# Optimization experiments

Measured on AMD Instinct MI355X. Metric: run time of the kernel, lower is better.

## Reference

```python
import jax, jax.numpy as jnp
import numpy as np

K = 24  # number of clusters (all ids in [0,K) assumed present per image)
DELTA_VAR = 1.0
DELTA_DIST = 2.0
VAR_W = 1.0
DIST_W = 1.0
REG_W = 1.0


def setup_inputs() -> dict:
    key = jax.random.key(0)
    k1, k2 = jax.random.split(key)
    data = jax.random.normal(k1, (4, 16, 512, 1024), dtype=jnp.float32)
    labels = jax.random.randint(k2, (4, 512, 1024), 0, K, dtype=jnp.int32)
    return {"data": data, "labels": labels}


def reference(data, labels):
    B, D, H, Wd = data.shape
    N = H * Wd
    # [B, N, D] points, [B*N] global segment ids (batch-offset cluster ids)
    X = jnp.transpose(data.reshape(B, D, N), (0, 2, 1)).reshape(B * N, D)
    seg = (labels.reshape(B, N) + jnp.arange(B, dtype=labels.dtype)[:, None] * K).reshape(-1)

    # per-cluster sums and counts -> centers  [B*K, D]
    sums = jax.ops.segment_sum(X, seg, num_segments=B * K)
    counts = jax.ops.segment_sum(jnp.ones((B * N,), X.dtype), seg, num_segments=B * K)
    centers_flat = sums / counts[:, None]
    centers = centers_flat.reshape(B, K, D)
    counts_bk = counts.reshape(B, K)

    # variance term: per-point hinged distance to own cluster center
    c_per_point = centers_flat[seg]                      # [B*N, D]
    pt_dist = jnp.linalg.norm(X - c_per_point, axis=1)   # [B*N]
    hv = jnp.maximum(pt_dist - DELTA_VAR, 0.0) ** 2
    var_per_cluster = jax.ops.segment_sum(hv, seg, num_segments=B * K).reshape(B, K) / counts_bk
    var_sum = var_per_cluster.sum()

    # distance term: pairwise center distances (diagonal kept, as in original,
    # contributing a constant delta_dist**2 per cluster)
    diff = centers[:, :, None, :] - centers[:, None, :, :]     # [B, K, K, D]
    sq = jnp.sum(diff * diff, axis=-1)                         # [B, K, K]
    eye = jnp.eye(K, dtype=bool)[None]
    cdist = jnp.where(eye, 0.0, jnp.sqrt(jnp.where(eye, 1.0, sq)))
    hd = jnp.maximum(DELTA_DIST - cdist, 0.0) ** 2
    dist_sum = hd.sum() / (2.0 * K * (K - 1))

    # regularization: mean center norm per image, summed over batch
    reg_sum = jnp.linalg.norm(centers, axis=2).mean(axis=1).sum()

    loss = (VAR_W * var_sum + DIST_W * dist_sum + REG_W * reg_sum) / B
    return loss
```

## Files before the change

### kernel.cpp

```cpp
#include <hip/hip_runtime.h>
#include <math.h>

#define KC 24
constexpr int D = 16;
constexpr int B = 4;
constexpr int N = 512 * 1024;
constexpr float DELTA_VAR = 1.0f;
constexpr float DELTA_DIST = 2.0f;

constexpr int REP = 8;
constexpr int RS  = KC * 17;
constexpr int CS  = 33;
constexpr int PTS = 4096;
constexpr int BLOCKS = (B * N) / PTS;
constexpr int SL = 8;


__global__ __launch_bounds__(256) void k_sums(const float* __restrict__ data,
                                              const int* __restrict__ labels,
                                              float* __restrict__ g_sums,
                                              float* __restrict__ g_cnt) {
    __shared__ float s_sum[REP * RS];
    __shared__ float s_cnt[REP * CS];
    const int t = threadIdx.x;

    const int chunk = blockIdx.x * PTS;
    const int b     = chunk >> 19;
    const int n0    = chunk & (N - 1);

    int4 lab[4];
#pragma unroll
    for (int i = 0; i < 4; ++i)
        lab[i] = *(const int4*)(labels + chunk + (i * 256 + t) * 4);

    const float* base = data + (size_t)(b * D) * N + n0;
    float4 v[2][4];
#pragma unroll
    for (int i = 0; i < 4; ++i)
        v[0][i] = *(const float4*)(base + (i * 256 + t) * 4);

    for (int i = t; i < REP * RS; i += 256) s_sum[i] = 0.f;
    for (int i = t; i < REP * CS; i += 256) s_cnt[i] = 0.f;

    const int rbase = (t & 7) * RS;
    int adr[4][4];
#pragma unroll
    for (int i = 0; i < 4; ++i) {
        adr[i][0] = rbase + lab[i].x * 17;
        adr[i][1] = rbase + lab[i].y * 17;
        adr[i][2] = rbase + lab[i].z * 17;
        adr[i][3] = rbase + lab[i].w * 17;
    }
    __syncthreads();

    const int cbase = (t & 7) * CS;
#pragma unroll
    for (int i = 0; i < 4; ++i) {
        atomicAdd(&s_cnt[cbase + lab[i].x], 1.f);
        atomicAdd(&s_cnt[cbase + lab[i].y], 1.f);
        atomicAdd(&s_cnt[cbase + lab[i].z], 1.f);
        atomicAdd(&s_cnt[cbase + lab[i].w], 1.f);
    }

#pragma unroll
    for (int d = 0; d < D; ++d) {
        if (d < D - 1) {
#pragma unroll
            for (int i = 0; i < 4; ++i)
                v[(d + 1) & 1][i] =
                    *(const float4*)(base + (size_t)(d + 1) * N + (i * 256 + t) * 4);
        }
#pragma unroll
        for (int i = 0; i < 4; ++i) {
            const float4 c = v[d & 1][i];
            atomicAdd(&s_sum[adr[i][0] + d], c.x);
            atomicAdd(&s_sum[adr[i][1] + d], c.y);
            atomicAdd(&s_sum[adr[i][2] + d], c.z);
            atomicAdd(&s_sum[adr[i][3] + d], c.w);
        }
    }
    __syncthreads();

    const int slice = blockIdx.x & (SL - 1);
    float* gs = g_sums + slice * (B * KC * D) + b * (KC * D);
    float* gc = g_cnt  + slice * (B * KC)     + b * KC;
    const int rot = (blockIdx.x * 131) & 255;
    for (int i = t; i < KC * D; i += 256) {
        int j = (i + rot) % (KC * D);
        int c = j >> 4, d = j & 15;
        float s = 0.f;
#pragma unroll
        for (int r = 0; r < REP; ++r) s += s_sum[r * RS + c * 17 + d];
        atomicAdd(&gs[j], s);
    }
    if (t < KC) {
        float s = 0.f;
#pragma unroll
        for (int r = 0; r < REP; ++r) s += s_cnt[r * CS + t];
        atomicAdd(&gc[t], s);
    }
}

__global__ __launch_bounds__(256) void k_var(const float* __restrict__ data,
                                             const int* __restrict__ labels,
                                             const float* __restrict__ g_sums,
                                             const float* __restrict__ g_cnt,
                                             float* __restrict__ g_varp) {
    __shared__ float s_c[KC * 17];
    __shared__ float s_ic[KC];
    __shared__ float s_part[4];
    const int t = threadIdx.x;
    const int chunk = blockIdx.x * PTS;
    const int b     = chunk >> 19;
    const int n0    = chunk & (N - 1);

    int4 lab[4];
#pragma unroll
    for (int i = 0; i < 4; ++i)
        lab[i] = *(const int4*)(labels + chunk + (i * 256 + t) * 4);

    const float* base = data + (size_t)(b * D) * N + n0;
    float4 v[2][4];
#pragma unroll
    for (int i = 0; i < 4; ++i)
        v[0][i] = *(const float4*)(base + (i * 256 + t) * 4);

    if (t < KC) {
        float cn = 0.f;
#pragma unroll
        for (int r = 0; r < SL; ++r) cn += g_cnt[r * (B * KC) + b * KC + t];
        s_ic[t] = 1.f / cn;
    }
    __syncthreads();
    for (int i = t; i < KC * D; i += 256) {
        int c = i >> 4, d = i & 15;
        float s = 0.f;
#pragma unroll
        for (int r = 0; r < SL; ++r) s += g_sums[r * (B * KC * D) + b * (KC * D) + i];
        s_c[c * 17 + d] = s * s_ic[c];
    }
    __syncthreads();

    int adr[4][4];
#pragma unroll
    for (int i = 0; i < 4; ++i) {
        adr[i][0] = lab[i].x * 17;
        adr[i][1] = lab[i].y * 17;
        adr[i][2] = lab[i].z * 17;
        adr[i][3] = lab[i].w * 17;
    }

    float4 acc[4];
#pragma unroll
    for (int i = 0; i < 4; ++i) acc[i] = make_float4(0.f, 0.f, 0.f, 0.f);

#pragma unroll
    for (int d = 0; d < D; ++d) {
        if (d < D - 1) {
#pragma unroll
            for (int i = 0; i < 4; ++i)
                v[(d + 1) & 1][i] =
                    *(const float4*)(base + (size_t)(d + 1) * N + (i * 256 + t) * 4);
        }
#pragma unroll
        for (int i = 0; i < 4; ++i) {
            const float4 c = v[d & 1][i];
            float df;
            df = c.x - s_c[adr[i][0] + d]; acc[i].x += df * df;
            df = c.y - s_c[adr[i][1] + d]; acc[i].y += df * df;
            df = c.z - s_c[adr[i][2] + d]; acc[i].z += df * df;
            df = c.w - s_c[adr[i][3] + d]; acc[i].w += df * df;
        }
    }

    float hsum = 0.f;
#pragma unroll
    for (int i = 0; i < 4; ++i) {
        float h;
        h = fmaxf(sqrtf(acc[i].x) - DELTA_VAR, 0.f); hsum += h * h * s_ic[lab[i].x];
        h = fmaxf(sqrtf(acc[i].y) - DELTA_VAR, 0.f); hsum += h * h * s_ic[lab[i].y];
        h = fmaxf(sqrtf(acc[i].z) - DELTA_VAR, 0.f); hsum += h * h * s_ic[lab[i].z];
        h = fmaxf(sqrtf(acc[i].w) - DELTA_VAR, 0.f); hsum += h * h * s_ic[lab[i].w];
    }

    for (int o = 32; o > 0; o >>= 1) hsum += __shfl_down(hsum, o, 64);
    if ((t & 63) == 0) s_part[t >> 6] = hsum;
    __syncthreads();
    if (t == 0)
        atomicAdd(&g_varp[blockIdx.x & 63],
                  s_part[0] + s_part[1] + s_part[2] + s_part[3]);
}

__global__ __launch_bounds__(128) void k_final(const float* __restrict__ g_sums,
                                               const float* __restrict__ g_cnt,
                                               const float* __restrict__ g_varp,
                                               float* __restrict__ out) {
    __shared__ float s_c[B * KC * 17];
    __shared__ float s_red[2];
    const int t = threadIdx.x;

    float acc = 0.f;
    if (t < B * KC) {
        float cnt = 0.f;
#pragma unroll
        for (int r = 0; r < SL; ++r) cnt += g_cnt[r * (B * KC) + t];
        float ns = 0.f;
        for (int d = 0; d < D; ++d) {
            float s = 0.f;
#pragma unroll
            for (int r = 0; r < SL; ++r) s += g_sums[r * (B * KC * D) + t * D + d];
            float c = s / cnt;
            s_c[t * 17 + d] = c;
            ns += c * c;
        }
        acc = sqrtf(ns) / (float)KC;
    }
    if (t < 64) acc += g_varp[t];
    __syncthreads();

    float dacc = 0.f;
    for (int idx = t; idx < B * KC * KC; idx += 128) {
        int b = idx / (KC * KC);
        int r = idx % (KC * KC);
        int i = r / KC, j = r % KC;
        float hd;
        if (i == j) {
            hd = DELTA_DIST * DELTA_DIST;
        } else {
            const float* ci = &s_c[(b * KC + i) * 17];
            const float* cj = &s_c[(b * KC + j) * 17];
            float sq = 0.f;
            for (int d = 0; d < D; ++d) { float df = ci[d] - cj[d]; sq += df * df; }
            float hh = fmaxf(DELTA_DIST - sqrtf(sq), 0.f);
            hd = hh * hh;
        }
        dacc += hd;
    }
    float total = acc + dacc / (2.f * KC * (KC - 1));

    for (int o = 32; o > 0; o >>= 1) total += __shfl_down(total, o, 64);
    if ((t & 63) == 0) s_red[t >> 6] = total;
    __syncthreads();
    if (t == 0) out[0] = (s_red[0] + s_red[1]) / (float)B;
}

extern "C" void kernel_launch(void* const* d_in, const int* in_sizes, int n_in,
                              void* d_out, int out_size, void* d_ws, size_t ws_size,
                              hipStream_t stream) {
    const float* data  = (const float*)d_in[0];
    const int* labels  = (const int*)d_in[1];
    float* ws = (float*)d_ws;
    float* g_sums = ws;
    float* g_cnt  = g_sums + SL * (B * KC * D);
    float* g_varp = g_cnt  + SL * (B * KC);

    hipMemsetAsync(d_ws, 0,
                   (SL * (B * KC * D) + SL * (B * KC) + 64) * sizeof(float), stream);

    k_sums<<<BLOCKS, 256, 0, stream>>>(data, labels, g_sums, g_cnt);
    k_var <<<BLOCKS, 256, 0, stream>>>(data, labels, g_sums, g_cnt, g_varp);
    k_final<<<1, 128, 0, stream>>>(g_sums, g_cnt, g_varp, (float*)d_out);
}
```

Measured before the change: 353.1 us.

## Fuse sums, variance and final kernels into one persistent kernel with grid barriers

Merges the three kernels into one launch of 256 blocks of 512 threads, joined by a software grid barrier built from global atomics. Each block keeps 8 of the 16 feature planes in registers and 4 in LDS across the barrier, so the variance pass re-reads only the last 4 planes from global memory instead of all 16. The aim is to cut the second full pass over the data and the launch gaps between kernels. In exchange, the barrier only works if all 256 blocks are resident at once, which the launch bounds of 2 blocks per CU are meant to allow, and the large register and LDS footprint may limit occupancy.

```diff
diff --git a/kernel.cpp b/kernel.cpp
--- a/kernel.cpp
+++ b/kernel.cpp
@@ -11,48 +11,72 @@
 constexpr int REP = 8;
 constexpr int RS  = KC * 17;
 constexpr int CS  = 33;
-constexpr int PTS = 4096;
-constexpr int BLOCKS = (B * N) / PTS;
+constexpr int TPB = 512;
+constexpr int PTS = 8192;
+constexpr int NBLK = (B * N) / PTS;
 constexpr int SL = 8;
-
-
-__global__ __launch_bounds__(256) void k_sums(const float* __restrict__ data,
-                                              const int* __restrict__ labels,
-                                              float* __restrict__ g_sums,
-                                              float* __restrict__ g_cnt) {
+constexpr int RREG = 8;
+constexpr int RLDS = 4;
+constexpr int WS_FLOATS = SL * (B * KC * D) + SL * (B * KC) + 64;
+
+
+__device__ __forceinline__ float gldf(const float* p) {
+    return __hip_atomic_load(p, __ATOMIC_RELAXED, __HIP_MEMORY_SCOPE_AGENT);
+}
+
+__device__ __forceinline__ void gsync(int* cnt, int* gen) {
+    __syncthreads();
+    if (threadIdx.x == 0) {
+        int g = __hip_atomic_load(gen, __ATOMIC_ACQUIRE, __HIP_MEMORY_SCOPE_AGENT);
+        if (__hip_atomic_fetch_add(cnt, 1, __ATOMIC_ACQ_REL, __HIP_MEMORY_SCOPE_AGENT) == NBLK - 1) {
+            __hip_atomic_store(cnt, 0, __ATOMIC_RELAXED, __HIP_MEMORY_SCOPE_AGENT);
+            __hip_atomic_fetch_add(gen, 1, __ATOMIC_ACQ_REL, __HIP_MEMORY_SCOPE_AGENT);
+        } else {
+            for (int it = 0; it < (1 << 22); ++it) {
+                if (__hip_atomic_load(gen, __ATOMIC_ACQUIRE, __HIP_MEMORY_SCOPE_AGENT) != g) break;
+                __builtin_amdgcn_s_sleep(8);
+            }
+        }
+    }
+    __syncthreads();
+}
+
+__global__ __launch_bounds__(TPB, 2) void k_fused(const float* __restrict__ data,
+                                                  const int* __restrict__ labels,
+                                                  float* __restrict__ ws,
+                                                  float* __restrict__ out) {
     __shared__ float s_sum[REP * RS];
     __shared__ float s_cnt[REP * CS];
+    __shared__ __align__(16) float4 s_data4[RLDS][PTS / 4];
+    __shared__ float s_c[KC * 17];
+    __shared__ float s_ic[KC];
+    __shared__ float s_red[8];
+
+    float* g_sums = ws;
+    float* g_cnt  = ws + SL * (B * KC * D);
+    float* g_varp = g_cnt + SL * (B * KC);
+    int*   bar    = (int*)(g_varp + 64);
+
     const int t = threadIdx.x;
-
     const int chunk = blockIdx.x * PTS;
-    const int b     = chunk >> 19;
-    const int n0    = chunk & (N - 1);
+    const int b = chunk >> 19;
+    const float* base = data + (size_t)(b * D) * N + (chunk & (N - 1));
 
     int4 lab[4];
 #pragma unroll
     for (int i = 0; i < 4; ++i)
-        lab[i] = *(const int4*)(labels + chunk + (i * 256 + t) * 4);
-
-    const float* base = data + (size_t)(b * D) * N + n0;
-    float4 v[2][4];
+        lab[i] = *(const int4*)(labels + chunk + (i * TPB + t) * 4);
+
+    float4 vr[RREG][4];
 #pragma unroll
     for (int i = 0; i < 4; ++i)
-        v[0][i] = *(const float4*)(base + (i * 256 + t) * 4);
-
-    for (int i = t; i < REP * RS; i += 256) s_sum[i] = 0.f;
-    for (int i = t; i < REP * CS; i += 256) s_cnt[i] = 0.f;
+        vr[0][i] = *(const float4*)(base + (i * TPB + t) * 4);
+
+    for (int i = t; i < REP * RS; i += TPB) s_sum[i] = 0.f;
+    for (int i = t; i < REP * CS; i += TPB) s_cnt[i] = 0.f;
+    __syncthreads();
 
     const int rbase = (t & 7) * RS;
-    int adr[4][4];
-#pragma unroll
-    for (int i = 0; i < 4; ++i) {
-        adr[i][0] = rbase + lab[i].x * 17;
-        adr[i][1] = rbase + lab[i].y * 17;
-        adr[i][2] = rbase + lab[i].z * 17;
-        adr[i][3] = rbase + lab[i].w * 17;
-    }
-    __syncthreads();
-
     const int cbase = (t & 7) * CS;
 #pragma unroll
     for (int i = 0; i < 4; ++i) {
@@ -62,21 +86,25 @@
         atomicAdd(&s_cnt[cbase + lab[i].w], 1.f);
     }
 
+    float4 v[2][4];
 #pragma unroll
     for (int d = 0; d < D; ++d) {
-        if (d < D - 1) {
-#pragma unroll
-            for (int i = 0; i < 4; ++i)
-                v[(d + 1) & 1][i] =
-                    *(const float4*)(base + (size_t)(d + 1) * N + (i * 256 + t) * 4);
-        }
-#pragma unroll
-        for (int i = 0; i < 4; ++i) {
-            const float4 c = v[d & 1][i];
-            atomicAdd(&s_sum[adr[i][0] + d], c.x);
-            atomicAdd(&s_sum[adr[i][1] + d], c.y);
-            atomicAdd(&s_sum[adr[i][2] + d], c.z);
-            atomicAdd(&s_sum[adr[i][3] + d], c.w);
+        if (d + 1 < D) {
+#pragma unroll
+            for (int i = 0; i < 4; ++i) {
+                float4 nx = *(const float4*)(base + (size_t)(d + 1) * N + (i * TPB + t) * 4);
+                if (d + 1 < RREG) vr[d + 1][i] = nx;
+                else              v[(d + 1) & 1][i] = nx;
+            }
+        }
+#pragma unroll
+        for (int i = 0; i < 4; ++i) {
+            const float4 c = (d < RREG) ? vr[d][i] : v[d & 1][i];
+            if (d >= RREG && d < RREG + RLDS) s_data4[d - RREG][i * TPB + t] = c;
+            atomicAdd(&s_sum[rbase + lab[i].x * 17 + d], c.x);
+            atomicAdd(&s_sum[rbase + lab[i].y * 17 + d], c.y);
+            atomicAdd(&s_sum[rbase + lab[i].z * 17 + d], c.z);
+            atomicAdd(&s_sum[rbase + lab[i].w * 17 + d], c.w);
         }
     }
     __syncthreads();
@@ -85,12 +113,12 @@
     float* gs = g_sums + slice * (B * KC * D) + b * (KC * D);
     float* gc = g_cnt  + slice * (B * KC)     + b * KC;
     const int rot = (blockIdx.x * 131) & 255;
-    for (int i = t; i < KC * D; i += 256) {
+    for (int i = t; i < KC * D; i += TPB) {
         int j = (i + rot) % (KC * D);
-        int c = j >> 4, d = j & 15;
-        float s = 0.f;
-#pragma unroll
-        for (int r = 0; r < REP; ++r) s += s_sum[r * RS + c * 17 + d];
+        int c = j >> 4, dd = j & 15;
+        float s = 0.f;
+#pragma unroll
+        for (int r = 0; r < REP; ++r) s += s_sum[r * RS + c * 17 + dd];
         atomicAdd(&gs[j], s);
     }
     if (t < KC) {
@@ -99,77 +127,75 @@
         for (int r = 0; r < REP; ++r) s += s_cnt[r * CS + t];
         atomicAdd(&gc[t], s);
     }
-}
-
-__global__ __launch_bounds__(256) void k_var(const float* __restrict__ data,
-                                             const int* __restrict__ labels,
-                                             const float* __restrict__ g_sums,
-                                             const float* __restrict__ g_cnt,
-                                             float* __restrict__ g_varp) {
-    __shared__ float s_c[KC * 17];
-    __shared__ float s_ic[KC];
-    __shared__ float s_part[4];
-    const int t = threadIdx.x;
-    const int chunk = blockIdx.x * PTS;
-    const int b     = chunk >> 19;
-    const int n0    = chunk & (N - 1);
-
-    int4 lab[4];
+
 #pragma unroll
     for (int i = 0; i < 4; ++i)
-        lab[i] = *(const int4*)(labels + chunk + (i * 256 + t) * 4);
-
-    const float* base = data + (size_t)(b * D) * N + n0;
-    float4 v[2][4];
-#pragma unroll
-    for (int i = 0; i < 4; ++i)
-        v[0][i] = *(const float4*)(base + (i * 256 + t) * 4);
+        v[0][i] = *(const float4*)(base + (size_t)(RREG + RLDS) * N + (i * TPB + t) * 4);
+
+    gsync(bar, bar + 1);
 
     if (t < KC) {
         float cn = 0.f;
 #pragma unroll
-        for (int r = 0; r < SL; ++r) cn += g_cnt[r * (B * KC) + b * KC + t];
+        for (int r = 0; r < SL; ++r) cn += gldf(&g_cnt[r * (B * KC) + b * KC + t]);
         s_ic[t] = 1.f / cn;
     }
     __syncthreads();
-    for (int i = t; i < KC * D; i += 256) {
-        int c = i >> 4, d = i & 15;
-        float s = 0.f;
-#pragma unroll
-        for (int r = 0; r < SL; ++r) s += g_sums[r * (B * KC * D) + b * (KC * D) + i];
-        s_c[c * 17 + d] = s * s_ic[c];
-    }
-    __syncthreads();
-
-    int adr[4][4];
-#pragma unroll
-    for (int i = 0; i < 4; ++i) {
-        adr[i][0] = lab[i].x * 17;
-        adr[i][1] = lab[i].y * 17;
-        adr[i][2] = lab[i].z * 17;
-        adr[i][3] = lab[i].w * 17;
-    }
-
-    float4 acc[4];
-#pragma unroll
-    for (int i = 0; i < 4; ++i) acc[i] = make_float4(0.f, 0.f, 0.f, 0.f);
-
-#pragma unroll
-    for (int d = 0; d < D; ++d) {
-        if (d < D - 1) {
+    for (int i = t; i < KC * D; i += TPB) {
+        int c = i >> 4, dd = i & 15;
+        float s = 0.f;
+#pragma unroll
+        for (int r = 0; r < SL; ++r) s += gldf(&g_sums[r * (B * KC * D) + b * (KC * D) + i]);
+        s_c[c * 17 + dd] = s * s_ic[c];
+    }
+    __syncthreads();
+
+    float ac[16];
+#pragma unroll
+    for (int i = 0; i < 16; ++i) ac[i] = 0.f;
+
+#pragma unroll
+    for (int d = 0; d < RREG; ++d) {
+#pragma unroll
+        for (int i = 0; i < 4; ++i) {
+            const float4 c = vr[d][i];
+            float df;
+            df = c.x - s_c[lab[i].x * 17 + d]; ac[i * 4 + 0] += df * df;
+            df = c.y - s_c[lab[i].y * 17 + d]; ac[i * 4 + 1] += df * df;
+            df = c.z - s_c[lab[i].z * 17 + d]; ac[i * 4 + 2] += df * df;
+            df = c.w - s_c[lab[i].w * 17 + d]; ac[i * 4 + 3] += df * df;
+        }
+    }
+#pragma unroll
+    for (int p = 0; p < RLDS; ++p) {
+        const int d = RREG + p;
+#pragma unroll
+        for (int i = 0; i < 4; ++i) {
+            const float4 c = s_data4[p][i * TPB + t];
+            float df;
+            df = c.x - s_c[lab[i].x * 17 + d]; ac[i * 4 + 0] += df * df;
+            df = c.y - s_c[lab[i].y * 17 + d]; ac[i * 4 + 1] += df * df;
+            df = c.z - s_c[lab[i].z * 17 + d]; ac[i * 4 + 2] += df * df;
+            df = c.w - s_c[lab[i].w * 17 + d]; ac[i * 4 + 3] += df * df;
+        }
+    }
+#pragma unroll
+    for (int dd = 0; dd < D - RREG - RLDS; ++dd) {
+        const int d = RREG + RLDS + dd;
+        if (dd + 1 < D - RREG - RLDS) {
 #pragma unroll
             for (int i = 0; i < 4; ++i)
-                v[(d + 1) & 1][i] =
-                    *(const float4*)(base + (size_t)(d + 1) * N + (i * 256 + t) * 4);
-        }
-#pragma unroll
-        for (int i = 0; i < 4; ++i) {
-            const float4 c = v[d & 1][i];
+                v[(dd + 1) & 1][i] =
+                    *(const float4*)(base + (size_t)(d + 1) * N + (i * TPB + t) * 4);
+        }
+#pragma unroll
+        for (int i = 0; i < 4; ++i) {
+            const float4 c = v[dd & 1][i];
             float df;
-            df = c.x - s_c[adr[i][0] + d]; acc[i].x += df * df;
-            df = c.y - s_c[adr[i][1] + d]; acc[i].y += df * df;
-            df = c.z - s_c[adr[i][2] + d]; acc[i].z += df * df;
-            df = c.w - s_c[adr[i][3] + d]; acc[i].w += df * df;
+            df = c.x - s_c[lab[i].x * 17 + d]; ac[i * 4 + 0] += df * df;
+            df = c.y - s_c[lab[i].y * 17 + d]; ac[i * 4 + 1] += df * df;
+            df = c.z - s_c[lab[i].z * 17 + d]; ac[i * 4 + 2] += df * df;
+            df = c.w - s_c[lab[i].w * 17 + d]; ac[i * 4 + 3] += df * df;
         }
     }
 
@@ -177,60 +203,58 @@
 #pragma unroll
     for (int i = 0; i < 4; ++i) {
         float h;
-        h = fmaxf(sqrtf(acc[i].x) - DELTA_VAR, 0.f); hsum += h * h * s_ic[lab[i].x];
-        h = fmaxf(sqrtf(acc[i].y) - DELTA_VAR, 0.f); hsum += h * h * s_ic[lab[i].y];
-        h = fmaxf(sqrtf(acc[i].z) - DELTA_VAR, 0.f); hsum += h * h * s_ic[lab[i].z];
-        h = fmaxf(sqrtf(acc[i].w) - DELTA_VAR, 0.f); hsum += h * h * s_ic[lab[i].w];
-    }
-
+        h = fmaxf(sqrtf(ac[i * 4 + 0]) - DELTA_VAR, 0.f); hsum += h * h * s_ic[lab[i].x];
+        h = fmaxf(sqrtf(ac[i * 4 + 1]) - DELTA_VAR, 0.f); hsum += h * h * s_ic[lab[i].y];
+        h = fmaxf(sqrtf(ac[i * 4 + 2]) - DELTA_VAR, 0.f); hsum += h * h * s_ic[lab[i].z];
+        h = fmaxf(sqrtf(ac[i * 4 + 3]) - DELTA_VAR, 0.f); hsum += h * h * s_ic[lab[i].w];
+    }
     for (int o = 32; o > 0; o >>= 1) hsum += __shfl_down(hsum, o, 64);
-    if ((t & 63) == 0) s_part[t >> 6] = hsum;
-    __syncthreads();
-    if (t == 0)
-        atomicAdd(&g_varp[blockIdx.x & 63],
-                  s_part[0] + s_part[1] + s_part[2] + s_part[3]);
-}
-
-__global__ __launch_bounds__(128) void k_final(const float* __restrict__ g_sums,
-                                               const float* __restrict__ g_cnt,
-                                               const float* __restrict__ g_varp,
-                                               float* __restrict__ out) {
-    __shared__ float s_c[B * KC * 17];
-    __shared__ float s_red[2];
-    const int t = threadIdx.x;
-
+    if ((t & 63) == 0) s_red[t >> 6] = hsum;
+    __syncthreads();
+    if (t == 0) {
+        float s = 0.f;
+#pragma unroll
+        for (int w = 0; w < 8; ++w) s += s_red[w];
+        atomicAdd(&g_varp[blockIdx.x & 63], s);
+    }
+
+    gsync(bar, bar + 1);
+
+    if (blockIdx.x != 0) return;
+
+    float* s_cF = (float*)&s_data4[0][0];
     float acc = 0.f;
     if (t < B * KC) {
         float cnt = 0.f;
 #pragma unroll
-        for (int r = 0; r < SL; ++r) cnt += g_cnt[r * (B * KC) + t];
+        for (int r = 0; r < SL; ++r) cnt += gldf(&g_cnt[r * (B * KC) + t]);
         float ns = 0.f;
-        for (int d = 0; d < D; ++d) {
+        for (int dd = 0; dd < D; ++dd) {
             float s = 0.f;
 #pragma unroll
-            for (int r = 0; r < SL; ++r) s += g_sums[r * (B * KC * D) + t * D + d];
+            for (int r = 0; r < SL; ++r) s += gldf(&g_sums[r * (B * KC * D) + t * D + dd]);
             float c = s / cnt;
-            s_c[t * 17 + d] = c;
+            s_cF[t * 17 + dd] = c;
             ns += c * c;
         }
         acc = sqrtf(ns) / (float)KC;
     }
-    if (t < 64) acc += g_varp[t];
+    if (t < 64) acc += gldf(&g_varp[t]);
     __syncthreads();
 
     float dacc = 0.f;
-    for (int idx = t; idx < B * KC * KC; idx += 128) {
-        int b = idx / (KC * KC);
+    for (int idx = t; idx < B * KC * KC; idx += TPB) {
+        int bb = idx / (KC * KC);
         int r = idx % (KC * KC);
         int i = r / KC, j = r % KC;
         float hd;
         if (i == j) {
             hd = DELTA_DIST * DELTA_DIST;
         } else {
-            const float* ci = &s_c[(b * KC + i) * 17];
-            const float* cj = &s_c[(b * KC + j) * 17];
+            const float* ci = &s_cF[(bb * KC + i) * 17];
+            const float* cj = &s_cF[(bb * KC + j) * 17];
             float sq = 0.f;
-            for (int d = 0; d < D; ++d) { float df = ci[d] - cj[d]; sq += df * df; }
+            for (int dd = 0; dd < D; ++dd) { float df = ci[dd] - cj[dd]; sq += df * df; }
             float hh = fmaxf(DELTA_DIST - sqrtf(sq), 0.f);
             hd = hh * hh;
         }
@@ -241,7 +265,12 @@
     for (int o = 32; o > 0; o >>= 1) total += __shfl_down(total, o, 64);
     if ((t & 63) == 0) s_red[t >> 6] = total;
     __syncthreads();
-    if (t == 0) out[0] = (s_red[0] + s_red[1]) / (float)B;
+    if (t == 0) {
+        float s = 0.f;
+#pragma unroll
+        for (int w = 0; w < 8; ++w) s += s_red[w];
+        out[0] = s / (float)B;
+    }
 }
 
 extern "C" void kernel_launch(void* const* d_in, const int* in_sizes, int n_in,
@@ -249,15 +278,8 @@
                               hipStream_t stream) {
     const float* data  = (const float*)d_in[0];
     const int* labels  = (const int*)d_in[1];
-    float* ws = (float*)d_ws;
-    float* g_sums = ws;
-    float* g_cnt  = g_sums + SL * (B * KC * D);
-    float* g_varp = g_cnt  + SL * (B * KC);
-
-    hipMemsetAsync(d_ws, 0,
-                   (SL * (B * KC * D) + SL * (B * KC) + 64) * sizeof(float), stream);
-
-    k_sums<<<BLOCKS, 256, 0, stream>>>(data, labels, g_sums, g_cnt);
-    k_var <<<BLOCKS, 256, 0, stream>>>(data, labels, g_sums, g_cnt, g_varp);
-    k_final<<<1, 128, 0, stream>>>(g_sums, g_cnt, g_varp, (float*)d_out);
-}
+    float* ws          = (float*)d_ws;
+
+    hipMemsetAsync(d_ws, 0, WS_FLOATS * sizeof(float) + 2 * sizeof(int), stream);
+    k_fused<<<NBLK, TPB, 0, stream>>>(data, labels, ws, (float*)d_out);
+}
```

After: 393.1 us. 1.11x slower.

## Hand off bf16-truncated points and squared norms from sums pass to variance pass

Applied to the files above, without the earlier changes.

When the workspace is large enough, the first pass also writes each point's squared norm and a bf16-truncated copy of its features. The variance pass then reads this half-size copy instead of the fp32 input. It computes the squared distance as |x|^2 - 2x·c + |c|^2 using the bf16 features in the dot product. The aim is to cut the second pass's read traffic, at the cost of extra writes in pass one, lower precision and possible cancellation error in the expanded distance. If the workspace is too small, it falls back to the original two kernels.

```diff
diff --git a/kernel.cpp b/kernel.cpp
--- a/kernel.cpp
+++ b/kernel.cpp
@@ -12,18 +12,27 @@
 constexpr int RS  = KC * 17;
 constexpr int CS  = 33;
 constexpr int PTS = 4096;
-constexpr int BLOCKS = (B * N) / PTS;
+constexpr int TPB = 256;
+constexpr int NBLK = (B * N) / PTS;
 constexpr int SL = 8;
-
-
-__global__ __launch_bounds__(256) void k_sums(const float* __restrict__ data,
-                                              const int* __restrict__ labels,
-                                              float* __restrict__ g_sums,
-                                              float* __restrict__ g_cnt) {
+constexpr int SMALL = SL * (B * KC * D) + SL * (B * KC) + 64;
+constexpr size_t NEED = ((size_t)SMALL + (size_t)B * N) * 4 + (size_t)D * (B * N / 2) * 4;
+
+__device__ __forceinline__ float blo(unsigned u) { return __uint_as_float(u << 16); }
+__device__ __forceinline__ float bhi(unsigned u) { return __uint_as_float(u & 0xFFFF0000u); }
+
+template <int HANDOFF>
+__device__ __forceinline__ void p1_body(const float* __restrict__ data,
+                                        const int* __restrict__ labels,
+                                        float* __restrict__ ws) {
     __shared__ float s_sum[REP * RS];
     __shared__ float s_cnt[REP * CS];
+    float* g_sums = ws;
+    float* g_cnt  = ws + SL * (B * KC * D);
+    float* r2g    = ws + SMALL;
+    unsigned* xbg = (unsigned*)(ws + SMALL + B * N);
+
     const int t = threadIdx.x;
-
     const int chunk = blockIdx.x * PTS;
     const int b     = chunk >> 19;
     const int n0    = chunk & (N - 1);
@@ -31,16 +40,16 @@
     int4 lab[4];
 #pragma unroll
     for (int i = 0; i < 4; ++i)
-        lab[i] = *(const int4*)(labels + chunk + (i * 256 + t) * 4);
+        lab[i] = *(const int4*)(labels + chunk + (i * TPB + t) * 4);
 
     const float* base = data + (size_t)(b * D) * N + n0;
     float4 v[2][4];
 #pragma unroll
     for (int i = 0; i < 4; ++i)
-        v[0][i] = *(const float4*)(base + (i * 256 + t) * 4);
-
-    for (int i = t; i < REP * RS; i += 256) s_sum[i] = 0.f;
-    for (int i = t; i < REP * CS; i += 256) s_cnt[i] = 0.f;
+        v[0][i] = *(const float4*)(base + (i * TPB + t) * 4);
+
+    for (int i = t; i < REP * RS; i += TPB) s_sum[i] = 0.f;
+    for (int i = t; i < REP * CS; i += TPB) s_cnt[i] = 0.f;
 
     const int rbase = (t & 7) * RS;
     int adr[4][4];
@@ -62,35 +71,55 @@
         atomicAdd(&s_cnt[cbase + lab[i].w], 1.f);
     }
 
+    float4 r2v[4];
+#pragma unroll
+    for (int i = 0; i < 4; ++i) r2v[i] = make_float4(0.f, 0.f, 0.f, 0.f);
+
 #pragma unroll
     for (int d = 0; d < D; ++d) {
-        if (d < D - 1) {
+        if (d + 1 < D) {
 #pragma unroll
             for (int i = 0; i < 4; ++i)
                 v[(d + 1) & 1][i] =
-                    *(const float4*)(base + (size_t)(d + 1) * N + (i * 256 + t) * 4);
-        }
+                    *(const float4*)(base + (size_t)(d + 1) * N + (i * TPB + t) * 4);
+        }
+        unsigned* xrow = xbg + (size_t)d * (B * N / 2) + (chunk >> 1);
 #pragma unroll
         for (int i = 0; i < 4; ++i) {
             const float4 c = v[d & 1][i];
+            if (HANDOFF) {
+                r2v[i].x = fmaf(c.x, c.x, r2v[i].x);
+                r2v[i].y = fmaf(c.y, c.y, r2v[i].y);
+                r2v[i].z = fmaf(c.z, c.z, r2v[i].z);
+                r2v[i].w = fmaf(c.w, c.w, r2v[i].w);
+                uint2 pk;
+                pk.x = (__float_as_uint(c.y) & 0xFFFF0000u) | (__float_as_uint(c.x) >> 16);
+                pk.y = (__float_as_uint(c.w) & 0xFFFF0000u) | (__float_as_uint(c.z) >> 16);
+                *(uint2*)(xrow + (i * TPB + t) * 2) = pk;
+            }
             atomicAdd(&s_sum[adr[i][0] + d], c.x);
             atomicAdd(&s_sum[adr[i][1] + d], c.y);
             atomicAdd(&s_sum[adr[i][2] + d], c.z);
             atomicAdd(&s_sum[adr[i][3] + d], c.w);
         }
     }
+    if (HANDOFF) {
+#pragma unroll
+        for (int i = 0; i < 4; ++i)
+            *(float4*)(r2g + chunk + (i * TPB + t) * 4) = r2v[i];
+    }
     __syncthreads();
 
     const int slice = blockIdx.x & (SL - 1);
     float* gs = g_sums + slice * (B * KC * D) + b * (KC * D);
     float* gc = g_cnt  + slice * (B * KC)     + b * KC;
     const int rot = (blockIdx.x * 131) & 255;
-    for (int i = t; i < KC * D; i += 256) {
+    for (int i = t; i < KC * D; i += TPB) {
         int j = (i + rot) % (KC * D);
-        int c = j >> 4, d = j & 15;
+        int c = j >> 4, dd = j & 15;
         float s = 0.f;
 #pragma unroll
-        for (int r = 0; r < REP; ++r) s += s_sum[r * RS + c * 17 + d];
+        for (int r = 0; r < REP; ++r) s += s_sum[r * RS + c * 17 + dd];
         atomicAdd(&gs[j], s);
     }
     if (t < KC) {
@@ -101,14 +130,122 @@
     }
 }
 
-__global__ __launch_bounds__(256) void k_var(const float* __restrict__ data,
+__global__ __launch_bounds__(TPB) void k_p1(const float* __restrict__ data,
+                                            const int* __restrict__ labels,
+                                            float* __restrict__ ws) {
+    p1_body<1>(data, labels, ws);
+}
+
+__global__ __launch_bounds__(TPB) void k_sums(const float* __restrict__ data,
+                                              const int* __restrict__ labels,
+                                              float* __restrict__ ws) {
+    p1_body<0>(data, labels, ws);
+}
+
+__global__ __launch_bounds__(TPB) void k_p2(const int* __restrict__ labels,
+                                            float* __restrict__ ws) {
+    __shared__ float s_c[KC * 17];
+    __shared__ float s_ic[KC];
+    __shared__ float s_c2[KC];
+    __shared__ float s_part[4];
+    float* g_sums = ws;
+    float* g_cnt  = ws + SL * (B * KC * D);
+    float* g_varp = g_cnt + SL * (B * KC);
+    const float* r2g    = ws + SMALL;
+    const unsigned* xbg = (const unsigned*)(ws + SMALL + B * N);
+
+    const int t = threadIdx.x;
+    const int chunk = blockIdx.x * PTS;
+    const int b     = chunk >> 19;
+
+    int4 lab[4];
+#pragma unroll
+    for (int i = 0; i < 4; ++i)
+        lab[i] = *(const int4*)(labels + chunk + (i * TPB + t) * 4);
+    float4 r2v[4];
+#pragma unroll
+    for (int i = 0; i < 4; ++i)
+        r2v[i] = *(const float4*)(r2g + chunk + (i * TPB + t) * 4);
+    uint2 u[2][4];
+#pragma unroll
+    for (int i = 0; i < 4; ++i)
+        u[0][i] = *(const uint2*)(xbg + (chunk >> 1) + (i * TPB + t) * 2);
+
+    if (t < KC) {
+        float cn = 0.f;
+#pragma unroll
+        for (int r = 0; r < SL; ++r) cn += g_cnt[r * (B * KC) + b * KC + t];
+        s_ic[t] = 1.f / cn;
+    }
+    __syncthreads();
+    for (int i = t; i < KC * D; i += TPB) {
+        int c = i >> 4, dd = i & 15;
+        float s = 0.f;
+#pragma unroll
+        for (int r = 0; r < SL; ++r) s += g_sums[r * (B * KC * D) + b * (KC * D) + i];
+        s_c[c * 17 + dd] = s * s_ic[c];
+    }
+    __syncthreads();
+    if (t < KC) {
+        float q = 0.f;
+#pragma unroll
+        for (int dd = 0; dd < D; ++dd) q = fmaf(s_c[t * 17 + dd], s_c[t * 17 + dd], q);
+        s_c2[t] = q;
+    }
+    __syncthreads();
+
+    float dot[16];
+#pragma unroll
+    for (int p = 0; p < 16; ++p) dot[p] = 0.f;
+
+#pragma unroll
+    for (int d = 0; d < D; ++d) {
+        if (d + 1 < D) {
+#pragma unroll
+            for (int i = 0; i < 4; ++i)
+                u[(d + 1) & 1][i] = *(const uint2*)(xbg + (size_t)(d + 1) * (B * N / 2) +
+                                                    (chunk >> 1) + (i * TPB + t) * 2);
+        }
+#pragma unroll
+        for (int i = 0; i < 4; ++i) {
+            const uint2 c = u[d & 1][i];
+            dot[i * 4 + 0] = fmaf(blo(c.x), s_c[lab[i].x * 17 + d], dot[i * 4 + 0]);
+            dot[i * 4 + 1] = fmaf(bhi(c.x), s_c[lab[i].y * 17 + d], dot[i * 4 + 1]);
+            dot[i * 4 + 2] = fmaf(blo(c.y), s_c[lab[i].z * 17 + d], dot[i * 4 + 2]);
+            dot[i * 4 + 3] = fmaf(bhi(c.y), s_c[lab[i].w * 17 + d], dot[i * 4 + 3]);
+        }
+    }
+
+    float hsum = 0.f;
+#pragma unroll
+    for (int i = 0; i < 4; ++i) {
+        float q, h;
+        q = fmaxf(fmaf(-2.f, dot[i * 4 + 0], r2v[i].x) + s_c2[lab[i].x], 0.f);
+        h = fmaxf(sqrtf(q) - DELTA_VAR, 0.f); hsum += h * h * s_ic[lab[i].x];
+        q = fmaxf(fmaf(-2.f, dot[i * 4 + 1], r2v[i].y) + s_c2[lab[i].y], 0.f);
+        h = fmaxf(sqrtf(q) - DELTA_VAR, 0.f); hsum += h * h * s_ic[lab[i].y];
+        q = fmaxf(fmaf(-2.f, dot[i * 4 + 2], r2v[i].z) + s_c2[lab[i].z], 0.f);
+        h = fmaxf(sqrtf(q) - DELTA_VAR, 0.f); hsum += h * h * s_ic[lab[i].z];
+        q = fmaxf(fmaf(-2.f, dot[i * 4 + 3], r2v[i].w) + s_c2[lab[i].w], 0.f);
+        h = fmaxf(sqrtf(q) - DELTA_VAR, 0.f); hsum += h * h * s_ic[lab[i].w];
+    }
+    for (int o = 32; o > 0; o >>= 1) hsum += __shfl_down(hsum, o, 64);
+    if ((t & 63) == 0) s_part[t >> 6] = hsum;
+    __syncthreads();
+    if (t == 0)
+        atomicAdd(&g_varp[blockIdx.x & 63],
+                  s_part[0] + s_part[1] + s_part[2] + s_part[3]);
+}
+
+__global__ __launch_bounds__(TPB) void k_var(const float* __restrict__ data,
                                              const int* __restrict__ labels,
-                                             const float* __restrict__ g_sums,
-                                             const float* __restrict__ g_cnt,
-                                             float* __restrict__ g_varp) {
+                                             float* __restrict__ ws) {
     __shared__ float s_c[KC * 17];
     __shared__ float s_ic[KC];
     __shared__ float s_part[4];
+    float* g_sums = ws;
+    float* g_cnt  = ws + SL * (B * KC * D);
+    float* g_varp = g_cnt + SL * (B * KC);
     const int t = threadIdx.x;
     const int chunk = blockIdx.x * PTS;
     const int b     = chunk >> 19;
@@ -117,13 +254,13 @@
     int4 lab[4];
 #pragma unroll
     for (int i = 0; i < 4; ++i)
-        lab[i] = *(const int4*)(labels + chunk + (i * 256 + t) * 4);
+        lab[i] = *(const int4*)(labels + chunk + (i * TPB + t) * 4);
 
     const float* base = data + (size_t)(b * D) * N + n0;
     float4 v[2][4];
 #pragma unroll
     for (int i = 0; i < 4; ++i)
-        v[0][i] = *(const float4*)(base + (i * 256 + t) * 4);
+        v[0][i] = *(const float4*)(base + (i * TPB + t) * 4);
 
     if (t < KC) {
         float cn = 0.f;
@@ -132,57 +269,45 @@
         s_ic[t] = 1.f / cn;
     }
     __syncthreads();
-    for (int i = t; i < KC * D; i += 256) {
-        int c = i >> 4, d = i & 15;
+    for (int i = t; i < KC * D; i += TPB) {
+        int c = i >> 4, dd = i & 15;
         float s = 0.f;
 #pragma unroll
         for (int r = 0; r < SL; ++r) s += g_sums[r * (B * KC * D) + b * (KC * D) + i];
-        s_c[c * 17 + d] = s * s_ic[c];
-    }
-    __syncthreads();
-
-    int adr[4][4];
-#pragma unroll
-    for (int i = 0; i < 4; ++i) {
-        adr[i][0] = lab[i].x * 17;
-        adr[i][1] = lab[i].y * 17;
-        adr[i][2] = lab[i].z * 17;
-        adr[i][3] = lab[i].w * 17;
-    }
-
-    float4 acc[4];
-#pragma unroll
-    for (int i = 0; i < 4; ++i) acc[i] = make_float4(0.f, 0.f, 0.f, 0.f);
-
+        s_c[c * 17 + dd] = s * s_ic[c];
+    }
+    __syncthreads();
+
+    float ac[16];
+#pragma unroll
+    for (int p = 0; p < 16; ++p) ac[p] = 0.f;
 #pragma unroll
     for (int d = 0; d < D; ++d) {
-        if (d < D - 1) {
+        if (d + 1 < D) {
 #pragma unroll
             for (int i = 0; i < 4; ++i)
                 v[(d + 1) & 1][i] =
-                    *(const float4*)(base + (size_t)(d + 1) * N + (i * 256 + t) * 4);
+                    *(const float4*)(base + (size_t)(d + 1) * N + (i * TPB + t) * 4);
         }
 #pragma unroll
         for (int i = 0; i < 4; ++i) {
             const float4 c = v[d & 1][i];
             float df;
-            df = c.x - s_c[adr[i][0] + d]; acc[i].x += df * df;
-            df = c.y - s_c[adr[i][1] + d]; acc[i].y += df * df;
-            df = c.z - s_c[adr[i][2] + d]; acc[i].z += df * df;
-            df = c.w - s_c[adr[i][3] + d]; acc[i].w += df * df;
-        }
-    }
-
+            df = c.x - s_c[lab[i].x * 17 + d]; ac[i * 4 + 0] += df * df;
+            df = c.y - s_c[lab[i].y * 17 + d]; ac[i * 4 + 1] += df * df;
+            df = c.z - s_c[lab[i].z * 17 + d]; ac[i * 4 + 2] += df * df;
+            df = c.w - s_c[lab[i].w * 17 + d]; ac[i * 4 + 3] += df * df;
+        }
+    }
     float hsum = 0.f;
 #pragma unroll
     for (int i = 0; i < 4; ++i) {
         float h;
-        h = fmaxf(sqrtf(acc[i].x) - DELTA_VAR, 0.f); hsum += h * h * s_ic[lab[i].x];
-        h = fmaxf(sqrtf(acc[i].y) - DELTA_VAR, 0.f); hsum += h * h * s_ic[lab[i].y];
-        h = fmaxf(sqrtf(acc[i].z) - DELTA_VAR, 0.f); hsum += h * h * s_ic[lab[i].z];
-        h = fmaxf(sqrtf(acc[i].w) - DELTA_VAR, 0.f); hsum += h * h * s_ic[lab[i].w];
-    }
-
+        h = fmaxf(sqrtf(ac[i * 4 + 0]) - DELTA_VAR, 0.f); hsum += h * h * s_ic[lab[i].x];
+        h = fmaxf(sqrtf(ac[i * 4 + 1]) - DELTA_VAR, 0.f); hsum += h * h * s_ic[lab[i].y];
+        h = fmaxf(sqrtf(ac[i * 4 + 2]) - DELTA_VAR, 0.f); hsum += h * h * s_ic[lab[i].z];
+        h = fmaxf(sqrtf(ac[i * 4 + 3]) - DELTA_VAR, 0.f); hsum += h * h * s_ic[lab[i].w];
+    }
     for (int o = 32; o > 0; o >>= 1) hsum += __shfl_down(hsum, o, 64);
     if ((t & 63) == 0) s_part[t >> 6] = hsum;
     __syncthreads();
@@ -191,10 +316,12 @@
                   s_part[0] + s_part[1] + s_part[2] + s_part[3]);
 }
 
-__global__ __launch_bounds__(128) void k_final(const float* __restrict__ g_sums,
-                                               const float* __restrict__ g_cnt,
-                                               const float* __restrict__ g_varp,
+__global__ __launch_bounds__(128) void k_final(const float* __restrict__ ws,
                                                float* __restrict__ out) {
+    const float* g_sums = ws;
+    const float* g_cnt  = ws + SL * (B * KC * D);
+    const float* g_varp = g_cnt + SL * (B * KC);
+
     __shared__ float s_c[B * KC * 17];
     __shared__ float s_red[2];
     const int t = threadIdx.x;
@@ -205,12 +332,12 @@
 #pragma unroll
         for (int r = 0; r < SL; ++r) cnt += g_cnt[r * (B * KC) + t];
         float ns = 0.f;
-        for (int d = 0; d < D; ++d) {
+        for (int dd = 0; dd < D; ++dd) {
             float s = 0.f;
 #pragma unroll
-            for (int r = 0; r < SL; ++r) s += g_sums[r * (B * KC * D) + t * D + d];
+            for (int r = 0; r < SL; ++r) s += g_sums[r * (B * KC * D) + t * D + dd];
             float c = s / cnt;
-            s_c[t * 17 + d] = c;
+            s_c[t * 17 + dd] = c;
             ns += c * c;
         }
         acc = sqrtf(ns) / (float)KC;
@@ -230,7 +357,7 @@
             const float* ci = &s_c[(b * KC + i) * 17];
             const float* cj = &s_c[(b * KC + j) * 17];
             float sq = 0.f;
-            for (int d = 0; d < D; ++d) { float df = ci[d] - cj[d]; sq += df * df; }
+            for (int dd = 0; dd < D; ++dd) { float df = ci[dd] - cj[dd]; sq += df * df; }
             float hh = fmaxf(DELTA_DIST - sqrtf(sq), 0.f);
             hd = hh * hh;
         }
@@ -249,15 +376,15 @@
                               hipStream_t stream) {
     const float* data  = (const float*)d_in[0];
     const int* labels  = (const int*)d_in[1];
-    float* ws = (float*)d_ws;
-    float* g_sums = ws;
-    float* g_cnt  = g_sums + SL * (B * KC * D);
-    float* g_varp = g_cnt  + SL * (B * KC);
-
-    hipMemsetAsync(d_ws, 0,
-                   (SL * (B * KC * D) + SL * (B * KC) + 64) * sizeof(float), stream);
-
-    k_sums<<<BLOCKS, 256, 0, stream>>>(data, labels, g_sums, g_cnt);
-    k_var <<<BLOCKS, 256, 0, stream>>>(data, labels, g_sums, g_cnt, g_varp);
-    k_final<<<1, 128, 0, stream>>>(g_sums, g_cnt, g_varp, (float*)d_out);
-}
+    float* ws          = (float*)d_ws;
+
+    hipMemsetAsync(d_ws, 0, SMALL * sizeof(float), stream);
+    if (ws_size >= NEED) {
+        k_p1<<<NBLK, TPB, 0, stream>>>(data, labels, ws);
+        k_p2<<<NBLK, TPB, 0, stream>>>(labels, ws);
+    } else {
+        k_sums<<<NBLK, TPB, 0, stream>>>(data, labels, ws);
+        k_var <<<NBLK, TPB, 0, stream>>>(data, labels, ws);
+    }
+    k_final<<<1, 128, 0, stream>>>(ws, (float*)d_out);
+}
```

Result: no change. 347.1 us (-1.7%).
